# Kernel optimization log

Measured on AMD Instinct MI355X. Metric: run time of the kernel, lower is better.

## Reference

```python
import jax, jax.numpy as jnp
import numpy as np

B, C, H, W = 2, 512, 48, 48
HEADS = 8          # head_dim = C // HEADS = 64
GROUPS = 32        # min(32, ceil(512/4)) = 32
EPS = 1e-5


def setup_inputs() -> dict:
    key = jax.random.key(0)
    ks = jax.random.split(key, 5)
    return {
        "x": jax.random.normal(ks[0], (B, C, H, W), jnp.float32),
        "gn_w": jnp.ones((C,), jnp.float32),
        "gn_b": jnp.zeros((C,), jnp.float32),
        # 1x1 convs stored as [out, in] matrices
        "qkv_w": jax.random.normal(ks[1], (3 * C, C), jnp.float32) / np.float32(np.sqrt(C)),
        "qkv_b": jax.random.normal(ks[2], (3 * C,), jnp.float32) * 0.01,
        "proj_w": jax.random.normal(ks[3], (C, C), jnp.float32) / np.float32(np.sqrt(C)),
        "proj_b": jax.random.normal(ks[4], (C,), jnp.float32) * 0.01,
    }


def _group_norm(x, w, b):
    b_, c_, h_, w_ = x.shape
    xg = x.reshape(b_, GROUPS, c_ // GROUPS, h_, w_)
    mean = xg.mean(axis=(2, 3, 4), keepdims=True)
    var = xg.var(axis=(2, 3, 4), keepdims=True)  # biased, matches F.group_norm
    xn = ((xg - mean) * jax.lax.rsqrt(var + EPS)).reshape(b_, c_, h_, w_)
    return xn * w[None, :, None, None] + b[None, :, None, None]


def reference(x, gn_w, gn_b, qkv_w, qkv_b, proj_w, proj_b):
    bx, cx, hx, wx = x.shape
    d = cx // HEADS
    n = hx * wx
    xn = _group_norm(x, gn_w, gn_b)
    # qkv 1x1 conv -> [B, 3C, H, W]
    y = jnp.einsum('oc,bchw->bohw', qkv_w, xn) + qkv_b[None, :, None, None]
    # torch: y.reshape(B*heads, d, 3, N).unbind(2)  (channel layout: head, chan, qkv)
    qkv = y.reshape(bx * HEADS, d, 3, n)
    q, k, v = qkv[:, :, 0, :], qkv[:, :, 1, :], qkv[:, :, 2, :]
    scale = np.float32(1.0 / np.sqrt(d))
    # AttentionOp: fp32 QK^T + softmax over keys (axis=2)
    w_attn = jax.nn.softmax(jnp.einsum('ncq,nck->nqk', q, k * scale), axis=2)
    a = jnp.einsum('nqk,nck->ncq', w_attn, v).reshape(bx, cx, hx, wx)
    out = jnp.einsum('oc,bchw->bohw', proj_w, a) + proj_b[None, :, None, None]
    return out + x
```

## Files before the change

### kernel.cpp

```cpp
#include <hip/hip_runtime.h>

typedef __bf16 bf16;
typedef __bf16 bf16x8 __attribute__((ext_vector_type(8)));
typedef __bf16 bf16x4 __attribute__((ext_vector_type(4)));
typedef float f32x4 __attribute__((ext_vector_type(4)));
typedef float f32x16 __attribute__((ext_vector_type(16)));

#define B_ 2
#define C_ 512
#define HW_ 2304
#define GROUPS_ 32
#define CPG_ 16
#define EPS_ 1e-5f
#define THR_ 8.0f
#define LOG2E_ 1.44269504f
#define EXP2(x) __builtin_amdgcn_exp2f(x)

__device__ __forceinline__ void gload_lds16(const bf16* g, bf16* l) {
  __builtin_amdgcn_global_load_lds((const __attribute__((address_space(1))) void*)g,
                                   (__attribute__((address_space(3))) void*)l, 16, 0, 0);
}

__global__ __launch_bounds__(256) void pre_k(const float* __restrict__ x,
                                             const float* __restrict__ qkv_w,
                                             const float* __restrict__ qkv_b,
                                             const float* __restrict__ proj_w,
                                             float* __restrict__ ps,
                                             float* __restrict__ pss,
                                             bf16* __restrict__ wqk,
                                             bf16* __restrict__ wv,
                                             bf16* __restrict__ wp,
                                             float* __restrict__ bqk,
                                             float* __restrict__ bv) {
  int blk = blockIdx.x;
  if (blk < 512) {
    int bg = blk >> 3, seg = blk & 7;
    const int n4 = CPG_ * HW_ / 4 / 8;
    const float4* p = (const float4*)(x + (long)bg * CPG_ * HW_) + (long)seg * n4;
    float s = 0.f, ss = 0.f;
    for (int i = threadIdx.x; i < n4; i += 256) {
      float4 v = p[i];
      s += v.x + v.y + v.z + v.w;
      ss += v.x * v.x + v.y * v.y + v.z * v.z + v.w * v.w;
    }
#pragma unroll
    for (int d = 1; d < 64; d <<= 1) { s += __shfl_xor(s, d); ss += __shfl_xor(ss, d); }
    __shared__ float rs[4], rss[4];
    int wave = threadIdx.x >> 6, lane = threadIdx.x & 63;
    if (lane == 0) { rs[wave] = s; rss[wave] = ss; }
    __syncthreads();
    if (threadIdx.x == 0) {
      ps[blk] = rs[0] + rs[1] + rs[2] + rs[3];
      pss[blk] = rss[0] + rss[1] + rss[2] + rss[3];
    }
  } else {
    int idx = (blk - 512) * 256 + threadIdx.x;
    int r = idx >> 9, c = idx & 511;
    {
      int src = (r < 512) ? 3 * r : 3 * (r - 512) + 1;
      float sc = (r < 512) ? 0.125f * LOG2E_ : 1.0f;
      wqk[idx] = (bf16)(qkv_w[(long)src * 512 + c] * sc);
    }
    if (r < 512) {
      wv[idx] = (bf16)(qkv_w[(long)(3 * r + 2) * 512 + c]);
      wp[idx] = (bf16)(proj_w[idx]);
    }
    if (idx < 1024) {
      int src = (idx < 512) ? 3 * idx : 3 * (idx - 512) + 1;
      float sc = (idx < 512) ? 0.125f * LOG2E_ : 1.0f;
      bqk[idx] = qkv_b[src] * sc;
    }
    if (idx < 512) bv[idx] = qkv_b[3 * idx + 2];
  }
}

__global__ __launch_bounds__(256) void gn_apply_k(const float* __restrict__ x,
                                                  const float* __restrict__ gw,
                                                  const float* __restrict__ gb,
                                                  const float* __restrict__ ps,
                                                  const float* __restrict__ pss,
                                                  bf16* __restrict__ xnT) {
  int n0 = blockIdx.x * 64, c0 = blockIdx.y * 32, b = blockIdx.z;
  int nn = n0 + (threadIdx.x & 63);
  int cb = c0 + ((threadIdx.x >> 6) << 3);
  int gi = b * GROUPS_ + (cb >> 4);
  float s = 0.f, ss = 0.f;
#pragma unroll
  for (int k = 0; k < 8; ++k) { s += ps[gi * 8 + k]; ss += pss[gi * 8 + k]; }
  const float invN = 1.0f / (float)(CPG_ * HW_);
  float mu = s * invN;
  float var = ss * invN - mu * mu;
  float rstd = rsqrtf(var + EPS_);
  bf16x8 o;
#pragma unroll
  for (int j = 0; j < 8; ++j) {
    int c = cb + j;
    float sc = rstd * gw[c];
    float sh = gb[c] - mu * sc;
    float v = x[((long)b * C_ + c) * HW_ + nn];
    o[j] = (bf16)(v * sc + sh);
  }
  *(bf16x8*)&xnT[((long)b * HW_ + nn) * C_ + cb] = o;
}

template <int BIAS_MODE, bool RESID, typename OUT_T>
__global__ __launch_bounds__(256) void gemm_k(const bf16* __restrict__ A,
                                              const bf16* __restrict__ BT,
                                              const float* __restrict__ bias,
                                              const float* __restrict__ resid,
                                              OUT_T* __restrict__ Cc,
                                              int M, int N,
                                              long sA, long sBT, long sC) {
  constexpr int KK = 512;
  constexpr int NSTEP = KK >> 6;
  int b = blockIdx.z;
  A += sA * b;
  BT += sBT * b;
  Cc += sC * b;
  const float* R = RESID ? (resid + sC * b) : nullptr;
  int m0 = blockIdx.y * 64, n0 = blockIdx.x * 64;
  int tid = threadIdx.x, lane = tid & 63, wave = tid >> 6;
  int wm = (wave >> 1) << 5, wn = (wave & 1) << 5;
  int fr = lane & 15, g = lane >> 4;
  __shared__ __align__(16) bf16 As[3][64 * 64];
  __shared__ __align__(16) bf16 Bs[3][64 * 64];
  int sr = tid >> 3;
  int swz = (((tid & 7) + sr) & 7) << 3;
  const bf16* gA = A + (long)(m0 + sr) * KK + swz;
  const bf16* gB = BT + (long)(n0 + sr) * KK + swz;
  int o0 = ((g - fr) & 7) << 3;
  int o1 = ((4 + g - fr) & 7) << 3;
  f32x4 acc[2][2] = {};
  gload_lds16(gA, &As[0][tid * 8]);
  gload_lds16(gA + 32 * KK, &As[0][2048 + tid * 8]);
  gload_lds16(gB, &Bs[0][tid * 8]);
  gload_lds16(gB + 32 * KK, &Bs[0][2048 + tid * 8]);
  gload_lds16(gA + 64, &As[1][tid * 8]);
  gload_lds16(gA + 32 * KK + 64, &As[1][2048 + tid * 8]);
  gload_lds16(gB + 64, &Bs[1][tid * 8]);
  gload_lds16(gB + 32 * KK + 64, &Bs[1][2048 + tid * 8]);
  asm volatile("s_waitcnt vmcnt(4)" ::: "memory");
  __builtin_amdgcn_s_barrier();
#pragma unroll
  for (int t = 0; t < NSTEP; ++t) {
    const int cur = t % 3;
    if (t + 2 < NSTEP) {
      const int nb = (t + 2) % 3;
      int k0 = (t + 2) << 6;
      gload_lds16(gA + k0, &As[nb][tid * 8]);
      gload_lds16(gA + 32 * KK + k0, &As[nb][2048 + tid * 8]);
      gload_lds16(gB + k0, &Bs[nb][tid * 8]);
      gload_lds16(gB + 32 * KK + k0, &Bs[nb][2048 + tid * 8]);
    }
    bf16x8 a00 = *(bf16x8*)&As[cur][(wm + fr) * 64 + o0];
    bf16x8 a01 = *(bf16x8*)&As[cur][(wm + fr) * 64 + o1];
    bf16x8 a10 = *(bf16x8*)&As[cur][(wm + 16 + fr) * 64 + o0];
    bf16x8 a11 = *(bf16x8*)&As[cur][(wm + 16 + fr) * 64 + o1];
    bf16x8 b00 = *(bf16x8*)&Bs[cur][(wn + fr) * 64 + o0];
    bf16x8 b01 = *(bf16x8*)&Bs[cur][(wn + fr) * 64 + o1];
    bf16x8 b10 = *(bf16x8*)&Bs[cur][(wn + 16 + fr) * 64 + o0];
    bf16x8 b11 = *(bf16x8*)&Bs[cur][(wn + 16 + fr) * 64 + o1];
    acc[0][0] = __builtin_amdgcn_mfma_f32_16x16x32_bf16(a00, b00, acc[0][0], 0, 0, 0);
    acc[0][0] = __builtin_amdgcn_mfma_f32_16x16x32_bf16(a01, b01, acc[0][0], 0, 0, 0);
    acc[0][1] = __builtin_amdgcn_mfma_f32_16x16x32_bf16(a00, b10, acc[0][1], 0, 0, 0);
    acc[0][1] = __builtin_amdgcn_mfma_f32_16x16x32_bf16(a01, b11, acc[0][1], 0, 0, 0);
    acc[1][0] = __builtin_amdgcn_mfma_f32_16x16x32_bf16(a10, b00, acc[1][0], 0, 0, 0);
    acc[1][0] = __builtin_amdgcn_mfma_f32_16x16x32_bf16(a11, b01, acc[1][0], 0, 0, 0);
    acc[1][1] = __builtin_amdgcn_mfma_f32_16x16x32_bf16(a10, b10, acc[1][1], 0, 0, 0);
    acc[1][1] = __builtin_amdgcn_mfma_f32_16x16x32_bf16(a11, b11, acc[1][1], 0, 0, 0);
    if (t + 2 < NSTEP) {
      asm volatile("s_waitcnt vmcnt(4) lgkmcnt(0)" ::: "memory");
    } else if (t + 1 < NSTEP) {
      asm volatile("s_waitcnt vmcnt(0) lgkmcnt(0)" ::: "memory");
    }
    if (t + 1 < NSTEP) __builtin_amdgcn_s_barrier();
  }
  int rbase = (lane >> 4) << 2;
#pragma unroll
  for (int mi = 0; mi < 2; ++mi)
#pragma unroll
    for (int nj = 0; nj < 2; ++nj)
#pragma unroll
      for (int reg = 0; reg < 4; ++reg) {
        int row = m0 + wm + (mi << 4) + rbase + reg;
        int col = n0 + wn + (nj << 4) + fr;
        float v = acc[mi][nj][reg];
        if (BIAS_MODE == 1) v += bias[row];
        if (BIAS_MODE == 2) v += bias[col];
        if (RESID) v += R[(long)row * N + col];
        Cc[(long)row * N + col] = (OUT_T)v;
      }
}

__global__ __launch_bounds__(256) void attn_k(const bf16* __restrict__ yT,
                                              const bf16* __restrict__ V,
                                              bf16* __restrict__ Op,
                                              float* __restrict__ Mp,
                                              float* __restrict__ Lp) {
  const int n = HW_;
  constexpr int NS = 2;
  constexpr int NT = (HW_ / NS) / 64;
  int bh = blockIdx.y, b = bh >> 3, head = bh & 7;
  int split = blockIdx.z;
  int q0 = blockIdx.x * 128;
  int kbeg = split * (n / NS);
  int tid = threadIdx.x, lane = tid & 63, wave = tid >> 6;
  int ql = lane & 31, hi = lane >> 5;
  const bf16* yTb = yT + (long)b * n * 1024;
  const bf16* Vb = V + ((long)b * C_ + head * 64) * n;
  const bf16* Kb = yTb + 512 + head * 64;

  int qrow = q0 + (wave << 5) + ql;
  const bf16* qp = yTb + (long)qrow * 1024 + head * 64 + (hi << 3);
  bf16x8 qf[4];
#pragma unroll
  for (int ds = 0; ds < 4; ++ds) qf[ds] = *(const bf16x8*)(qp + (ds << 4));

  __shared__ __align__(16) bf16 Kt[2][64][64];
  __shared__ __align__(16) bf16 Vt[2][64][64];

  int rotb = hi + (lane & 7);

  float m_run = -1e30f, l_run = 0.f;
  f32x16 oacc0 = {}, oacc1 = {};

  int r0 = tid >> 3;
  int ck = tid & 7;
  int c0e = ck << 3;
  int pk = ((ck + r0) & 7) << 3;
  int kl0 = (c0e & 48) | ((c0e & 8) >> 1);
  int pv0 = ((((kl0 >> 3) + r0) & 7) << 3) | (kl0 & 7);
  int pv1 = ((((kl0 >> 3) + 1 + r0) & 7) << 3) | (kl0 & 7);

  const bf16* kptr = Kb + (long)(kbeg + r0) * 1024 + c0e;
  const bf16* vptr = Vb + (long)r0 * n + kbeg + c0e;
  uint4 rk0 = *(const uint4*)kptr;
  uint4 rk1 = *(const uint4*)(kptr + 32 * 1024);
  uint4 rv0 = *(const uint4*)vptr;
  uint4 rv1 = *(const uint4*)(vptr + 32 * n);
  *(uint4*)&Kt[0][r0][pk] = rk0;
  *(uint4*)&Kt[0][r0 + 32][pk] = rk1;
  *(uint2*)&Vt[0][r0][pv0] = make_uint2(rv0.x, rv0.y);
  *(uint2*)&Vt[0][r0][pv1] = make_uint2(rv0.z, rv0.w);
  *(uint2*)&Vt[0][r0 + 32][pv0] = make_uint2(rv1.x, rv1.y);
  *(uint2*)&Vt[0][r0 + 32][pv1] = make_uint2(rv1.z, rv1.w);
  kptr += 64 * 1024;
  vptr += 64;
  rk0 = *(const uint4*)kptr;
  rk1 = *(const uint4*)(kptr + 32 * 1024);
  rv0 = *(const uint4*)vptr;
  rv1 = *(const uint4*)(vptr + 32 * n);
  __syncthreads();

  for (int t = 0; t < NT; ++t) {
    int cur = t & 1;
    f32x16 s0 = {}, s1 = {};
    __builtin_amdgcn_s_setprio(1);
#pragma unroll
    for (int ds = 0; ds < 4; ++ds) {
      int off = (((ds << 1) + rotb) & 7) << 3;
      bf16x8 kf0 = *(bf16x8*)&Kt[cur][ql][off];
      bf16x8 kf1 = *(bf16x8*)&Kt[cur][32 + ql][off];
      s0 = __builtin_amdgcn_mfma_f32_32x32x16_bf16(kf0, qf[ds], s0, 0, 0, 0);
      s1 = __builtin_amdgcn_mfma_f32_32x32x16_bf16(kf1, qf[ds], s1, 0, 0, 0);
    }
    __builtin_amdgcn_s_setprio(0);
    if (t + 1 < NT) {
      int nb = cur ^ 1;
      *(uint4*)&Kt[nb][r0][pk] = rk0;
      *(uint4*)&Kt[nb][r0 + 32][pk] = rk1;
      *(uint2*)&Vt[nb][r0][pv0] = make_uint2(rv0.x, rv0.y);
      *(uint2*)&Vt[nb][r0][pv1] = make_uint2(rv0.z, rv0.w);
      *(uint2*)&Vt[nb][r0 + 32][pv0] = make_uint2(rv1.x, rv1.y);
      *(uint2*)&Vt[nb][r0 + 32][pv1] = make_uint2(rv1.z, rv1.w);
      if (t + 2 < NT) {
        kptr += 64 * 1024;
        vptr += 64;
        rk0 = *(const uint4*)kptr;
        rk1 = *(const uint4*)(kptr + 32 * 1024);
        rv0 = *(const uint4*)vptr;
        rv1 = *(const uint4*)(vptr + 32 * n);
      }
    }
    float pm = fmaxf(s0[0], s1[0]);
#pragma unroll
    for (int r = 1; r < 16; ++r) pm = fmaxf(pm, fmaxf(s0[r], s1[r]));
    pm = fmaxf(pm, __shfl_xor(pm, 32));
    if (__any(pm > m_run + THR_)) {
      float mn = fmaxf(m_run, pm);
      float corr = EXP2(m_run - mn);
      m_run = mn;
      l_run *= corr;
#pragma unroll
      for (int r = 0; r < 16; ++r) { oacc0[r] *= corr; oacc1[r] *= corr; }
    }
    float ls = 0.f;
    bf16x8 pa[2][2];
#pragma unroll
    for (int r = 0; r < 16; ++r) {
      float p0 = EXP2(s0[r] - m_run);
      float p1 = EXP2(s1[r] - m_run);
      ls += p0 + p1;
      pa[0][r >> 3][r & 7] = (bf16)p0;
      pa[1][r >> 3][r & 7] = (bf16)p1;
    }
    ls += __shfl_xor(ls, 32);
    l_run += ls;
    __builtin_amdgcn_s_setprio(1);
#pragma unroll
    for (int m = 0; m < 2; ++m)
#pragma unroll
      for (int sl = 0; sl < 2; ++sl) {
        int off = (((m << 2) + (sl << 1) + rotb) & 7) << 3;
        bf16x8 vf0 = *(bf16x8*)&Vt[cur][ql][off];
        bf16x8 vf1 = *(bf16x8*)&Vt[cur][32 + ql][off];
        oacc0 = __builtin_amdgcn_mfma_f32_32x32x16_bf16(vf0, pa[m][sl], oacc0, 0, 0, 0);
        oacc1 = __builtin_amdgcn_mfma_f32_32x32x16_bf16(vf1, pa[m][sl], oacc1, 0, 0, 0);
      }
    __builtin_amdgcn_s_setprio(0);
    __syncthreads();
  }
  long orow = (long)(split * 16 + bh) * n + q0 + (wave << 5) + ql;
#pragma unroll
  for (int rg = 0; rg < 4; ++rg) {
    bf16x4 ov0 = {(bf16)oacc0[rg * 4 + 0], (bf16)oacc0[rg * 4 + 1],
                  (bf16)oacc0[rg * 4 + 2], (bf16)oacc0[rg * 4 + 3]};
    bf16x4 ov1 = {(bf16)oacc1[rg * 4 + 0], (bf16)oacc1[rg * 4 + 1],
                  (bf16)oacc1[rg * 4 + 2], (bf16)oacc1[rg * 4 + 3]};
    *(bf16x4*)&Op[orow * 64 + (rg << 3) + (hi << 2)] = ov0;
    *(bf16x4*)&Op[orow * 64 + 32 + (rg << 3) + (hi << 2)] = ov1;
  }
  if (hi == 0) {
    Mp[orow] = m_run;
    Lp[orow] = l_run;
  }
}

template <int NS>
__global__ __launch_bounds__(256) void attn_merge_k(const bf16* __restrict__ Op,
                                                    const float* __restrict__ Mp,
                                                    const float* __restrict__ Lp,
                                                    bf16* __restrict__ aT) {
  int bh = blockIdx.y, b = bh >> 3, h = bh & 7;
  int gi = blockIdx.x * 256 + threadIdx.x;
  int nrow = gi >> 3, dd8 = (gi & 7) << 3;
  long idx[NS];
  float mm = -1e30f;
#pragma unroll
  for (int s = 0; s < NS; ++s) {
    idx[s] = (long)(s * 16 + bh) * HW_ + nrow;
    mm = fmaxf(mm, Mp[idx[s]]);
  }
  float l = 0.f, w[NS];
#pragma unroll
  for (int s = 0; s < NS; ++s) {
    w[s] = EXP2(Mp[idx[s]] - mm);
    l += Lp[idx[s]] * w[s];
  }
  float invl = 1.f / l;
  float oaccf[8] = {};
#pragma unroll
  for (int s = 0; s < NS; ++s) {
    bf16x8 o = *(const bf16x8*)&Op[idx[s] * 64 + dd8];
    float ws = w[s] * invl;
#pragma unroll
    for (int j = 0; j < 8; ++j) oaccf[j] += (float)o[j] * ws;
  }
  bf16x8 o;
#pragma unroll
  for (int j = 0; j < 8; ++j) o[j] = (bf16)oaccf[j];
  *(bf16x8*)&aT[((long)b * HW_ + nrow) * C_ + h * 64 + dd8] = o;
}

extern "C" void kernel_launch(void* const* d_in, const int* in_sizes, int n_in,
                              void* d_out, int out_size, void* d_ws, size_t ws_size,
                              hipStream_t stream) {
  const float* x = (const float*)d_in[0];
  const float* gn_w = (const float*)d_in[1];
  const float* gn_b = (const float*)d_in[2];
  const float* qkv_w = (const float*)d_in[3];
  const float* qkv_b = (const float*)d_in[4];
  const float* proj_w = (const float*)d_in[5];
  const float* proj_b = (const float*)d_in[6];
  float* out = (float*)d_out;

  char* ws = (char*)d_ws;
  float* ps = (float*)ws;   ws += 2048;
  float* pss = (float*)ws;  ws += 2048;
  float* bqk = (float*)ws;  ws += 4096;
  float* bv = (float*)ws;   ws += 2048;
  bf16* wqk = (bf16*)ws;    ws += 1024l * 512 * 2;
  bf16* wv = (bf16*)ws;     ws += 512l * 512 * 2;
  bf16* wp = (bf16*)ws;     ws += 512l * 512 * 2;
  bf16* xnT = (bf16*)ws;    ws += 2l * HW_ * 512 * 2;
  bf16* yT = (bf16*)ws;     ws += 2l * HW_ * 1024 * 2;
  bf16* v = (bf16*)ws;      ws += 2l * 512 * HW_ * 2;
  bf16* aT = (bf16*)ws;     ws += 2l * HW_ * 512 * 2;
  bf16* Op = (bf16*)ws;     ws += 2l * 16 * HW_ * 64 * 2;
  float* Mp = (float*)ws;   ws += 2l * 16 * HW_ * 4;
  float* Lp = (float*)ws;   ws += 2l * 16 * HW_ * 4;

  pre_k<<<2560, 256, 0, stream>>>(x, qkv_w, qkv_b, proj_w, ps, pss, wqk, wv, wp, bqk, bv);
  gn_apply_k<<<dim3(36, 16, 2), 256, 0, stream>>>(x, gn_w, gn_b, ps, pss, xnT);
  gemm_k<2, false, bf16><<<dim3(16, 36, 2), 256, 0, stream>>>(
      xnT, wqk, bqk, nullptr, yT, 2304, 1024, (long)HW_ * 512, 0, (long)HW_ * 1024);
  gemm_k<1, false, bf16><<<dim3(36, 8, 2), 256, 0, stream>>>(
      wv, xnT, bv, nullptr, v, 512, 2304, 0, (long)HW_ * 512, 512l * HW_);
  attn_k<<<dim3(18, 16, 2), 256, 0, stream>>>(yT, v, Op, Mp, Lp);
  attn_merge_k<2><<<dim3(72, 16), 256, 0, stream>>>(Op, Mp, Lp, aT);
  gemm_k<1, true, float><<<dim3(36, 8, 2), 256, 0, stream>>>(
      wp, aT, proj_b, x, out, 512, 2304, 0, (long)HW_ * 512, 512l * HW_);
}
```

Before: 93.50 us.

## Template attention key-split count, use four splits when workspace allows

The attention kernel is templated on the number of key splits, and the host picks four splits instead of two when the workspace is large enough. This doubles the attention grid from 576 to 1152 blocks so more CUs stay busy. The cost is more partial output to write and merge. The V tile loading is also reworked to fetch two 8-byte chunks per row and store them as one 16-byte swizzled LDS write instead of two split writes.

Result: faster. 89.05 us (-4.8%).

```diff
diff --git a/kernel.cpp b/kernel.cpp
--- a/kernel.cpp
+++ b/kernel.cpp
@@ -192,13 +192,13 @@
       }
 }
 
+template <int NS>
 __global__ __launch_bounds__(256) void attn_k(const bf16* __restrict__ yT,
                                               const bf16* __restrict__ V,
                                               bf16* __restrict__ Op,
                                               float* __restrict__ Mp,
                                               float* __restrict__ Lp) {
   const int n = HW_;
-  constexpr int NS = 2;
   constexpr int NT = (HW_ / NS) / 64;
   int bh = blockIdx.y, b = bh >> 3, head = bh & 7;
   int split = blockIdx.z;
@@ -228,28 +228,28 @@
   int ck = tid & 7;
   int c0e = ck << 3;
   int pk = ((ck + r0) & 7) << 3;
-  int kl0 = (c0e & 48) | ((c0e & 8) >> 1);
-  int pv0 = ((((kl0 >> 3) + r0) & 7) << 3) | (kl0 & 7);
-  int pv1 = ((((kl0 >> 3) + 1 + r0) & 7) << 3) | (kl0 & 7);
+  int K0 = ((ck & 4) << 3) | ((ck & 2) << 3) | ((ck & 1) << 2);
 
   const bf16* kptr = Kb + (long)(kbeg + r0) * 1024 + c0e;
-  const bf16* vptr = Vb + (long)r0 * n + kbeg + c0e;
+  const bf16* vptr = Vb + (long)r0 * n + kbeg + K0;
   uint4 rk0 = *(const uint4*)kptr;
   uint4 rk1 = *(const uint4*)(kptr + 32 * 1024);
-  uint4 rv0 = *(const uint4*)vptr;
-  uint4 rv1 = *(const uint4*)(vptr + 32 * n);
+  uint2 va0 = *(const uint2*)vptr;
+  uint2 vb0 = *(const uint2*)(vptr + 8);
+  uint2 va1 = *(const uint2*)(vptr + 32 * n);
+  uint2 vb1 = *(const uint2*)(vptr + 32 * n + 8);
   *(uint4*)&Kt[0][r0][pk] = rk0;
   *(uint4*)&Kt[0][r0 + 32][pk] = rk1;
-  *(uint2*)&Vt[0][r0][pv0] = make_uint2(rv0.x, rv0.y);
-  *(uint2*)&Vt[0][r0][pv1] = make_uint2(rv0.z, rv0.w);
-  *(uint2*)&Vt[0][r0 + 32][pv0] = make_uint2(rv1.x, rv1.y);
-  *(uint2*)&Vt[0][r0 + 32][pv1] = make_uint2(rv1.z, rv1.w);
+  *(uint4*)&Vt[0][r0][pk] = make_uint4(va0.x, va0.y, vb0.x, vb0.y);
+  *(uint4*)&Vt[0][r0 + 32][pk] = make_uint4(va1.x, va1.y, vb1.x, vb1.y);
   kptr += 64 * 1024;
   vptr += 64;
   rk0 = *(const uint4*)kptr;
   rk1 = *(const uint4*)(kptr + 32 * 1024);
-  rv0 = *(const uint4*)vptr;
-  rv1 = *(const uint4*)(vptr + 32 * n);
+  va0 = *(const uint2*)vptr;
+  vb0 = *(const uint2*)(vptr + 8);
+  va1 = *(const uint2*)(vptr + 32 * n);
+  vb1 = *(const uint2*)(vptr + 32 * n + 8);
   __syncthreads();
 
   for (int t = 0; t < NT; ++t) {
@@ -269,17 +269,17 @@
       int nb = cur ^ 1;
       *(uint4*)&Kt[nb][r0][pk] = rk0;
       *(uint4*)&Kt[nb][r0 + 32][pk] = rk1;
-      *(uint2*)&Vt[nb][r0][pv0] = make_uint2(rv0.x, rv0.y);
-      *(uint2*)&Vt[nb][r0][pv1] = make_uint2(rv0.z, rv0.w);
-      *(uint2*)&Vt[nb][r0 + 32][pv0] = make_uint2(rv1.x, rv1.y);
-      *(uint2*)&Vt[nb][r0 + 32][pv1] = make_uint2(rv1.z, rv1.w);
+      *(uint4*)&Vt[nb][r0][pk] = make_uint4(va0.x, va0.y, vb0.x, vb0.y);
+      *(uint4*)&Vt[nb][r0 + 32][pk] = make_uint4(va1.x, va1.y, vb1.x, vb1.y);
       if (t + 2 < NT) {
         kptr += 64 * 1024;
         vptr += 64;
         rk0 = *(const uint4*)kptr;
         rk1 = *(const uint4*)(kptr + 32 * 1024);
-        rv0 = *(const uint4*)vptr;
-        rv1 = *(const uint4*)(vptr + 32 * n);
+        va0 = *(const uint2*)vptr;
+        vb0 = *(const uint2*)(vptr + 8);
+        va1 = *(const uint2*)(vptr + 32 * n);
+        vb1 = *(const uint2*)(vptr + 32 * n + 8);
       }
     }
     float pm = fmaxf(s0[0], s1[0]);
@@ -396,9 +396,13 @@
   bf16* yT = (bf16*)ws;     ws += 2l * HW_ * 1024 * 2;
   bf16* v = (bf16*)ws;      ws += 2l * 512 * HW_ * 2;
   bf16* aT = (bf16*)ws;     ws += 2l * HW_ * 512 * 2;
-  bf16* Op = (bf16*)ws;     ws += 2l * 16 * HW_ * 64 * 2;
-  float* Mp = (float*)ws;   ws += 2l * 16 * HW_ * 4;
-  float* Lp = (float*)ws;   ws += 2l * 16 * HW_ * 4;
+  bf16* Op = (bf16*)ws;
+  size_t base_used = (size_t)(ws - (char*)d_ws);
+  size_t need4 = base_used + 4ull * 16 * HW_ * 64 * 2 + 2ull * 4 * 16 * HW_ * 4;
+  int NS = (ws_size >= need4) ? 4 : 2;
+  ws += (size_t)NS * 16 * HW_ * 64 * 2;
+  float* Mp = (float*)ws;   ws += (size_t)NS * 16 * HW_ * 4;
+  float* Lp = (float*)ws;   ws += (size_t)NS * 16 * HW_ * 4;
 
   pre_k<<<2560, 256, 0, stream>>>(x, qkv_w, qkv_b, proj_w, ps, pss, wqk, wv, wp, bqk, bv);
   gn_apply_k<<<dim3(36, 16, 2), 256, 0, stream>>>(x, gn_w, gn_b, ps, pss, xnT);
@@ -406,8 +410,13 @@
       xnT, wqk, bqk, nullptr, yT, 2304, 1024, (long)HW_ * 512, 0, (long)HW_ * 1024);
   gemm_k<1, false, bf16><<<dim3(36, 8, 2), 256, 0, stream>>>(
       wv, xnT, bv, nullptr, v, 512, 2304, 0, (long)HW_ * 512, 512l * HW_);
-  attn_k<<<dim3(18, 16, 2), 256, 0, stream>>>(yT, v, Op, Mp, Lp);
-  attn_merge_k<2><<<dim3(72, 16), 256, 0, stream>>>(Op, Mp, Lp, aT);
+  if (NS == 4) {
+    attn_k<4><<<dim3(18, 16, 4), 256, 0, stream>>>(yT, v, Op, Mp, Lp);
+    attn_merge_k<4><<<dim3(72, 16), 256, 0, stream>>>(Op, Mp, Lp, aT);
+  } else {
+    attn_k<2><<<dim3(18, 16, 2), 256, 0, stream>>>(yT, v, Op, Mp, Lp);
+    attn_merge_k<2><<<dim3(72, 16), 256, 0, stream>>>(Op, Mp, Lp, aT);
+  }
   gemm_k<1, true, float><<<dim3(36, 8, 2), 256, 0, stream>>>(
       wp, aT, proj_b, x, out, 512, 2304, 0, (long)HW_ * 512, 512l * HW_);
 }
```
